# Kernel optimization log

Hardware: AMD Instinct MI355X
Metric: run time of the kernel (lower is better)

## Reference

```python
import jax, jax.numpy as jnp
import numpy as np

N_HEADS = 16
ROPE_BASE = 10000.0


def _apply_rope(t, cos, sin):
    # t: (B, H, S, D); cos/sin: (S, D/2). Rotate-half convention.
    d2 = t.shape[-1] // 2
    t1, t2 = t[..., :d2], t[..., d2:]
    return jnp.concatenate([t1 * cos - t2 * sin, t2 * cos + t1 * sin], axis=-1)


def setup_inputs() -> dict:
    key = jax.random.key(0)
    k0, k1, k2, k3, k4 = jax.random.split(key, 5)
    B, S, E = 4, 2048, 1024
    scale = 0.02
    x = jax.random.normal(k0, (B, S, E), dtype=jnp.float32)
    w_qkv = jax.random.normal(k1, (E, 3 * E), dtype=jnp.float32) * scale
    b_qkv = jnp.zeros((3 * E,), dtype=jnp.float32)
    w_proj = jax.random.normal(k2, (E, E), dtype=jnp.float32) * scale
    b_proj = jnp.zeros((E,), dtype=jnp.float32)
    return {"x": x, "w_qkv": w_qkv, "b_qkv": b_qkv, "w_proj": w_proj, "b_proj": b_proj}


def reference(x, w_qkv, b_qkv, w_proj, b_proj):
    B, S, E = x.shape
    H = N_HEADS
    D = E // H
    # fused QKV projection
    qkv = x @ w_qkv + b_qkv                      # (B, S, 3E)
    q, k, v = jnp.split(qkv, 3, axis=-1)
    def to_heads(t):
        return t.reshape(B, S, H, D).transpose(0, 2, 1, 3)  # (B, H, S, D)
    q, k, v = to_heads(q), to_heads(k), to_heads(v)
    # RoPE (rotate-half)
    inv_freq = ROPE_BASE ** (-jnp.arange(0, D, 2, dtype=jnp.float32) / D)  # (D/2,)
    pos = jnp.arange(S, dtype=jnp.float32)
    freqs = pos[:, None] * inv_freq[None, :]     # (S, D/2)
    cos, sin = jnp.cos(freqs), jnp.sin(freqs)
    q = _apply_rope(q, cos, sin)
    k = _apply_rope(k, cos, sin)
    # causal SDPA
    scores = jnp.einsum('bhqd,bhkd->bhqk', q, k) / jnp.sqrt(jnp.float32(D))
    causal = jnp.tril(jnp.ones((S, S), dtype=bool))
    scores = jnp.where(causal, scores, jnp.float32(-1e30))
    probs = jax.nn.softmax(scores, axis=-1)
    out = jnp.einsum('bhqk,bhkd->bhqd', probs, v)  # (B, H, S, D)
    out = out.transpose(0, 2, 1, 3).reshape(B, S, E)
    # output projection (dropout is identity at p=0 / eval)
    return out @ w_proj + b_proj
```

## Files before the change

kernel.cpp:

```cpp
#include <hip/hip_runtime.h>

typedef unsigned short u16;
typedef __bf16 bf16x8 __attribute__((ext_vector_type(8)));
typedef float f32x4 __attribute__((ext_vector_type(4)));

__device__ __forceinline__ u16 f2b(float f) {
    unsigned u = __builtin_bit_cast(unsigned, f);
    unsigned r = (u + 0x7fffu + ((u >> 16) & 1u)) >> 16;
    return (u16)r;
}
#if __has_builtin(__builtin_amdgcn_cvt_pk_bf16_f32)
typedef __bf16 bf16x2_t __attribute__((ext_vector_type(2)));
__device__ __forceinline__ unsigned pk2(float a, float b) {
    return __builtin_bit_cast(unsigned, __builtin_amdgcn_cvt_pk_bf16_f32(a, b));
}
#else
__device__ __forceinline__ unsigned pk2(float a, float b) {
    return (unsigned)f2b(a) | ((unsigned)f2b(b) << 16);
}
#endif
#if __has_builtin(__builtin_amdgcn_exp2f)
#define EXP2F(x) __builtin_amdgcn_exp2f(x)
#else
#define EXP2F(x) exp2f(x)
#endif

__device__ __forceinline__ void gl_lds16(const u16* g, u16* l) {
    __builtin_amdgcn_global_load_lds(
        (const __attribute__((address_space(1))) unsigned*)(const void*)g,
        (__attribute__((address_space(3))) unsigned*)(void*)l, 16, 0, 0);
}

__device__ __forceinline__ void transpose64(const float* __restrict__ in,
                                            u16* __restrict__ out, int R, int C,
                                            int tr, int tc, int tid, u16 (*tile)[66]) {
    for (int i = tid; i < 4096; i += 256) {
        int r = i >> 6, c = i & 63;
        tile[c][r] = f2b(in[(size_t)(tr + r) * C + tc + c]);
    }
    __syncthreads();
    for (int i = tid; i < 4096; i += 256) {
        int r = i >> 6, c = i & 63;
        out[(size_t)(tc + r) * R + tr + c] = tile[r][c];
    }
}

__global__ __launch_bounds__(256) void k_prep(const float* __restrict__ x,
                                              u16* __restrict__ x_bf,
                                              const float* __restrict__ w_qkv,
                                              u16* __restrict__ wqkvT,
                                              const float* __restrict__ w_proj,
                                              u16* __restrict__ wprojT,
                                              float2* __restrict__ tab) {
    __shared__ u16 tile[64][66];
    int bid = blockIdx.x, tid = threadIdx.x;
    if (bid < 4096) {
        int i = bid * 256 + tid;
        const float4* p = (const float4*)(x + (size_t)i * 8);
        float4 a = p[0], b = p[1];
        u16 t[8] = {f2b(a.x), f2b(a.y), f2b(a.z), f2b(a.w),
                    f2b(b.x), f2b(b.y), f2b(b.z), f2b(b.w)};
        *(uint4*)(x_bf + (size_t)i * 8) = *(const uint4*)t;
    } else if (bid < 4864) {
        int q = bid - 4096;
        transpose64(w_qkv, wqkvT, 1024, 3072, (q / 48) * 64, (q % 48) * 64, tid, tile);
    } else if (bid < 5120) {
        int q = bid - 4864;
        transpose64(w_proj, wprojT, 1024, 1024, (q / 16) * 64, (q % 16) * 64, tid, tile);
    } else {
        int i = (bid - 5120) * 256 + tid;
        int s = i >> 5, d = i & 31;
        const float C0 = 0.4152410118609203f;
        float inv_freq = exp2f(-C0 * (float)d);
        float sn, cs;
        sincosf((float)s * inv_freq, &sn, &cs);
        tab[i] = make_float2(cs, sn);
    }
}

__device__ __forceinline__ void gemm_mainloop(const u16* __restrict__ Ab,
                                              const u16* __restrict__ Bb, int K,
                                              u16* As, u16* Bs, int tid,
                                              f32x4 (&acc)[4][4]) {
    const int wave = tid >> 6, lane = tid & 63;
    const int col = lane & 15, quad = lane >> 4;
    const int wm = wave >> 1, wn = wave & 1;
    const int lrow = lane >> 2, lk = (lane & 3) * 8;
    u16* ldsA0 = As + (wave * 16) * 32;
    u16* ldsA1 = As + (64 + wave * 16) * 32;
    u16* ldsB0 = Bs + (wave * 16) * 32;
    u16* ldsB1 = Bs + (64 + wave * 16) * 32;
    const u16* gA0 = Ab + (size_t)(wave * 16 + lrow) * K + lk;
    const u16* gA1 = gA0 + (size_t)64 * K;
    const u16* gB0 = Bb + (size_t)(wave * 16 + lrow) * K + lk;
    const u16* gB1 = gB0 + (size_t)64 * K;
    for (int k0 = 0; k0 < K; k0 += 64) {
        if (k0) __syncthreads();
#pragma unroll
        for (int kh = 0; kh < 2; ++kh) {
            int ko = k0 + kh * 32;
            gl_lds16(gA0 + ko, ldsA0 + kh * 4096);
            gl_lds16(gA1 + ko, ldsA1 + kh * 4096);
            gl_lds16(gB0 + ko, ldsB0 + kh * 4096);
            gl_lds16(gB1 + ko, ldsB1 + kh * 4096);
        }
        __syncthreads();
#pragma unroll
        for (int kh = 0; kh < 2; ++kh) {
            bf16x8 af[4], bfr[4];
#pragma unroll
            for (int mt = 0; mt < 4; ++mt)
                af[mt] = *(const bf16x8*)(As + kh * 4096 +
                                          (wm * 64 + mt * 16 + col) * 32 + quad * 8);
#pragma unroll
            for (int nt = 0; nt < 4; ++nt)
                bfr[nt] = *(const bf16x8*)(Bs + kh * 4096 +
                                           (wn * 64 + nt * 16 + col) * 32 + quad * 8);
#pragma unroll
            for (int mt = 0; mt < 4; ++mt)
#pragma unroll
                for (int nt = 0; nt < 4; ++nt)
                    acc[mt][nt] = __builtin_amdgcn_mfma_f32_16x16x32_bf16(
                        af[mt], bfr[nt], acc[mt][nt], 0, 0, 0);
        }
    }
}

__global__ __launch_bounds__(256) void k_gemm_qkv_rope(
    const u16* __restrict__ A, const u16* __restrict__ Bt,
    const float* __restrict__ bias, const float2* __restrict__ tab,
    u16* __restrict__ Qr, u16* __restrict__ Kr, u16* __restrict__ Vt) {
    __shared__ __align__(16) u16 smem[16384];
    u16* As = smem;
    u16* Bs = smem + 8192;
    const int K = 1024;
    int tid = threadIdx.x;
    int lane = tid & 63, wave = tid >> 6;
    int col = lane & 15, quad = lane >> 4;
    int wm = wave >> 1, wn = wave & 1;
    int mBase = blockIdx.y * 128;
    int nBase = blockIdx.x * 128;
    f32x4 acc[4][4] = {};
    gemm_mainloop(A + (size_t)mBase * K, Bt + (size_t)nBase * K, K, As, Bs, tid, acc);

    int region = nBase >> 10;
    int n64 = nBase + wn * 64;
    int h = (n64 & 1023) >> 6;
    if (region < 2) {
        __syncthreads();
        float qs = (region == 0) ? 0.18033688011112042f : 1.0f;
#pragma unroll
        for (int nt = 0; nt < 2; ++nt) {
            int d1 = nt * 16 + col;
            float b1 = bias[n64 + d1];
            float b2 = bias[n64 + d1 + 32];
            int nl = wn * 64 + nt * 16 + col;
#pragma unroll
            for (int mt = 0; mt < 4; ++mt) {
                int mlb = wm * 64 + mt * 16 + quad * 4;
#pragma unroll
                for (int r = 0; r < 4; ++r) {
                    int mloc = mlb + r;
                    int s = (mBase + mloc) & 2047;
                    float2 t = tab[s * 32 + d1];
                    float t1 = acc[mt][nt][r] + b1;
                    float t2 = acc[mt][nt + 2][r] + b2;
                    int sw = (mloc & 7) << 3;
                    smem[mloc * 128 + (nl ^ sw)] = f2b((t1 * t.x - t2 * t.y) * qs);
                    smem[mloc * 128 + ((nl + 32) ^ sw)] = f2b((t2 * t.x + t1 * t.y) * qs);
                }
            }
        }
        __syncthreads();
        u16* outp = (region == 0) ? Qr : Kr;
#pragma unroll
        for (int p = 0; p < 8; ++p) {
            int lin = p * 256 + tid;
            int mloc = lin >> 4;
            int c8 = (lin & 15) << 3;
            uint4 v = *(const uint4*)(smem + mloc * 128 + (c8 ^ ((mloc & 7) << 3)));
            int m = mBase + mloc;
            int s = m & 2047, b = m >> 11;
            int ng = (nBase & 1023) + c8;
            *(uint4*)(outp + ((size_t)((b * 16 + (ng >> 6)) * 2048 + s)) * 64 +
                      (ng & 63)) = v;
        }
    } else {
        int b = mBase >> 11;
        int sb0 = mBase & 2047;
#pragma unroll
        for (int nt = 0; nt < 4; ++nt) {
            int d = nt * 16 + col;
            float bv = bias[n64 + d];
            u16* vrow = Vt + ((size_t)((b * 16 + h) * 64 + d)) * 2048;
#pragma unroll
            for (int mt = 0; mt < 4; ++mt) {
                int s = sb0 + wm * 64 + mt * 16 + quad * 4;
                uint2 w;
                w.x = pk2(acc[mt][nt][0] + bv, acc[mt][nt][1] + bv);
                w.y = pk2(acc[mt][nt][2] + bv, acc[mt][nt][3] + bv);
                *(uint2*)(vrow + s) = w;
            }
        }
    }
}

__device__ __forceinline__ void stage_kv(const u16* __restrict__ Kt,
                                         const u16* __restrict__ Vtb, u16* KsB,
                                         u16* VsB, int wave, int lane) {
    int lr = lane >> 3;
    int lc = lane & 7;
#pragma unroll
    for (int i = 0; i < 2; ++i) {
        int s = wave * 2 + i;
        int r = s * 8 + lr;
        int key = (r & 3) | (((r >> 3) & 1) << 2);
        gl_lds16(Kt + (size_t)r * 64 + ((lc ^ key) << 3), KsB + s * 512);
    }
#pragma unroll
    for (int i = 0; i < 2; ++i) {
        int s = wave * 2 + i;
        int d = s * 8 + lr;
        int key = d & 7;
        gl_lds16(Vtb + (size_t)d * 2048 + ((lc ^ key) << 3), VsB + s * 512);
    }
}

__global__ __launch_bounds__(256, 4) void k_attn(const u16* __restrict__ Qr,
                                                 const u16* __restrict__ Kr,
                                                 const u16* __restrict__ Vt,
                                                 u16* __restrict__ O) {
    __shared__ __align__(16) u16 Ks[2][4096];
    __shared__ __align__(16) u16 Vs[2][4096];
    int tid = threadIdx.x, wave = tid >> 6, lane = tid & 63;
    int col = lane & 15, quad = lane >> 4;
    int id = blockIdx.x + (blockIdx.y << 4);
    int xcd = id & 7, w = id >> 3;
    int head = xcd * 8 + (w & 7);
    int tsel = w >> 3;
    int b = head >> 4, h = head & 15;
    size_t headQ = (size_t)head * 2048 * 64;
    size_t headV = (size_t)head * 64 * 2048;
    int prow = (col >> 2) * 8 + (col & 3);
    int ck = col & 7;

#pragma unroll 1
    for (int phase = 0; phase < 2; ++phase) {
        int T = phase ? tsel : 31 - tsel;
        int myq = T * 64 + wave * 16 + col;
        const u16* qp = Qr + headQ + (size_t)myq * 64;
        bf16x8 aq0 = *(const bf16x8*)(qp + quad * 8);
        bf16x8 aq1 = *(const bf16x8*)(qp + 32 + quad * 8);
        f32x4 o[4] = {};
        float l = 0.f;

        stage_kv(Kr + headQ, Vt + headV, Ks[0], Vs[0], wave, lane);
        __syncthreads();

        for (int j = 0; j <= T; ++j) {
            int cur = j & 1;
            if (j < T)
                stage_kv(Kr + headQ + ((size_t)(j + 1) << 12),
                         Vt + headV + (j + 1) * 64, Ks[cur ^ 1], Vs[cur ^ 1],
                         wave, lane);
            const u16* KsC = Ks[cur];
            const u16* VsC = Vs[cur];
            f32x4 s[4];
            __builtin_amdgcn_s_setprio(1);
#pragma unroll
            for (int nt = 0; nt < 4; ++nt) {
                const u16* kp = KsC + ((nt & 1) * 32 + (nt >> 1) * 4 + prow) * 64;
                bf16x8 ak0 = *(const bf16x8*)(kp + ((quad ^ ck) << 3));
                bf16x8 ak1 = *(const bf16x8*)(kp + (((quad + 4) ^ ck) << 3));
                f32x4 z = {};
                z = __builtin_amdgcn_mfma_f32_16x16x32_bf16(ak0, aq0, z, 0, 0, 0);
                s[nt] = __builtin_amdgcn_mfma_f32_16x16x32_bf16(ak1, aq1, z, 0, 0, 0);
            }
            __builtin_amdgcn_s_setprio(0);
            if (j == T) {
#pragma unroll
                for (int nt = 0; nt < 4; ++nt) {
                    int keyb = j * 64 + (nt & 1) * 32 + quad * 8 + (nt >> 1) * 4;
#pragma unroll
                    for (int r = 0; r < 4; ++r)
                        if (keyb + r > myq) s[nt][r] = -3.0e38f;
                }
            }
            unsigned P4[8];
#pragma unroll
            for (int nt = 0; nt < 4; ++nt) {
                float p0 = EXP2F(s[nt][0]);
                float p1 = EXP2F(s[nt][1]);
                float p2 = EXP2F(s[nt][2]);
                float p3 = EXP2F(s[nt][3]);
                l += (p0 + p1) + (p2 + p3);
                P4[2 * nt] = pk2(p0, p1);
                P4[2 * nt + 1] = pk2(p2, p3);
            }
            __builtin_amdgcn_s_setprio(1);
#pragma unroll
            for (int kk = 0; kk < 2; ++kk) {
                uint4 bw;
                bw.x = P4[2 * kk];
                bw.y = P4[2 * kk + 1];
                bw.z = P4[2 * kk + 4];
                bw.w = P4[2 * kk + 5];
                bf16x8 bp = __builtin_bit_cast(bf16x8, bw);
#pragma unroll
                for (int mt = 0; mt < 4; ++mt) {
                    bf16x8 av = *(const bf16x8*)(VsC + (mt * 16 + col) * 64 +
                                                 (((kk * 4 + quad) ^ ck) << 3));
                    o[mt] = __builtin_amdgcn_mfma_f32_16x16x32_bf16(av, bp, o[mt], 0, 0, 0);
                }
            }
            __builtin_amdgcn_s_setprio(0);
            __syncthreads();
        }
        l += __shfl_xor(l, 16);
        l += __shfl_xor(l, 32);
        float inv = 1.0f / l;
        u16* orow = O + (size_t)(b * 2048 + myq) * 1024 + h * 64;
#pragma unroll
        for (int mt = 0; mt < 4; ++mt) {
            uint2 w2;
            w2.x = pk2(o[mt][0] * inv, o[mt][1] * inv);
            w2.y = pk2(o[mt][2] * inv, o[mt][3] * inv);
            *(uint2*)(orow + mt * 16 + quad * 4) = w2;
        }
    }
}

__device__ __forceinline__ void proj_mainloop(const u16* __restrict__ Ab,
                                              const u16* __restrict__ Bb,
                                              u16* As, u16* Bs, int tid,
                                              f32x4 (&acc)[2][4]) {
    const int wave = tid >> 6, lane = tid & 63;
    const int col = lane & 15, quad = lane >> 4;
    const int lrow = lane >> 2, lk = (lane & 3) * 8;
    u16* ldsA0 = As + (wave * 16) * 32;
    u16* ldsA1 = As + (64 + wave * 16) * 32;
    u16* ldsB0 = Bs + (wave * 16) * 32;
    const u16* gA0 = Ab + (size_t)(wave * 16 + lrow) * 1024 + lk;
    const u16* gA1 = gA0 + (size_t)64 * 1024;
    const u16* gB0 = Bb + (size_t)(wave * 16 + lrow) * 1024 + lk;
    for (int k0 = 0; k0 < 1024; k0 += 64) {
        if (k0) __syncthreads();
#pragma unroll
        for (int kh = 0; kh < 2; ++kh) {
            int ko = k0 + kh * 32;
            gl_lds16(gA0 + ko, ldsA0 + kh * 4096);
            gl_lds16(gA1 + ko, ldsA1 + kh * 4096);
            gl_lds16(gB0 + ko, ldsB0 + kh * 2048);
        }
        __syncthreads();
#pragma unroll
        for (int kh = 0; kh < 2; ++kh) {
            bf16x8 af[2], bfr[4];
#pragma unroll
            for (int mt = 0; mt < 2; ++mt)
                af[mt] = *(const bf16x8*)(As + kh * 4096 +
                                          (wave * 32 + mt * 16 + col) * 32 + quad * 8);
#pragma unroll
            for (int nt = 0; nt < 4; ++nt)
                bfr[nt] = *(const bf16x8*)(Bs + kh * 2048 +
                                           (nt * 16 + col) * 32 + quad * 8);
#pragma unroll
            for (int mt = 0; mt < 2; ++mt)
#pragma unroll
                for (int nt = 0; nt < 4; ++nt)
                    acc[mt][nt] = __builtin_amdgcn_mfma_f32_16x16x32_bf16(
                        af[mt], bfr[nt], acc[mt][nt], 0, 0, 0);
        }
    }
}

__global__ __launch_bounds__(256, 4) void k_gemm_proj(const u16* __restrict__ A,
                                                      const u16* __restrict__ Bt,
                                                      const float* __restrict__ bias,
                                                      float* __restrict__ out) {
    __shared__ __align__(16) u16 As[2 * 128 * 32];
    __shared__ __align__(16) u16 Bs[2 * 64 * 32];
    int tid = threadIdx.x;
    int lane = tid & 63, wave = tid >> 6;
    int col = lane & 15, quad = lane >> 4;
    int mBase = blockIdx.y * 128;
    int nBase = blockIdx.x * 64;
    f32x4 acc[2][4] = {};
    proj_mainloop(A + (size_t)mBase * 1024, Bt + (size_t)nBase * 1024, As, Bs, tid, acc);
#pragma unroll
    for (int nt = 0; nt < 4; ++nt) {
        int n = nBase + nt * 16 + col;
        float bv = bias[n];
#pragma unroll
        for (int mt = 0; mt < 2; ++mt) {
            int m = mBase + wave * 32 + mt * 16 + quad * 4;
#pragma unroll
            for (int r = 0; r < 4; ++r)
                out[(size_t)(m + r) * 1024 + n] = acc[mt][nt][r] + bv;
        }
    }
}

extern "C" void kernel_launch(void* const* d_in, const int* in_sizes, int n_in,
                              void* d_out, int out_size, void* d_ws, size_t ws_size,
                              hipStream_t stream) {
    const float* x = (const float*)d_in[0];
    const float* w_qkv = (const float*)d_in[1];
    const float* b_qkv = (const float*)d_in[2];
    const float* w_proj = (const float*)d_in[3];
    const float* b_proj = (const float*)d_in[4];
    float* out = (float*)d_out;
    char* ws = (char*)d_ws;
    u16* x_bf = (u16*)(ws);
    u16* wqkvT = (u16*)(ws + 16777216);
    u16* wprojT = (u16*)(ws + 23068672);
    u16* Qr = (u16*)(ws + 25165824);
    u16* Kr = (u16*)(ws + 41943040);
    u16* Vt = (u16*)(ws + 58720256);
    u16* AO = (u16*)(ws + 75497472);
    float2* tab = (float2*)(ws + 75497472);

    k_prep<<<5376, 256, 0, stream>>>(x, x_bf, w_qkv, wqkvT, w_proj, wprojT, tab);
    k_gemm_qkv_rope<<<dim3(24, 64), 256, 0, stream>>>(x_bf, wqkvT, b_qkv, tab, Qr, Kr, Vt);
    k_attn<<<dim3(16, 64), 256, 0, stream>>>(Qr, Kr, Vt, AO);
    k_gemm_proj<<<dim3(16, 64), 256, 0, stream>>>(AO, wprojT, b_proj, out);
}
```

Baseline: 254.3 us.

## Triple-buffer K tiles in attention and replace syncthreads with vmcnt-gated barriers

Splits the K/V staging helper into separate K and V loaders and grows the K LDS buffer from two to three slots, so K is prefetched two tiles ahead while V stays one tile ahead. Full __syncthreads is replaced by explicit s_waitcnt vmcnt counts plus raw s_barrier and sched_barrier. The V wait now sits just before the PV MFMAs, so the QK and softmax work can overlap the outstanding V loads. This adds LDS use, which may lower occupancy. The V wait only covers each wave's own global-to-LDS loads and has no barrier before other waves read them, so there is a cross-wave race risk.

```diff
diff --git a/kernel.cpp b/kernel.cpp
--- a/kernel.cpp
+++ b/kernel.cpp
@@ -205,11 +205,9 @@
     }
 }
 
-__device__ __forceinline__ void stage_kv(const u16* __restrict__ Kt,
-                                         const u16* __restrict__ Vtb, u16* KsB,
-                                         u16* VsB, int wave, int lane) {
-    int lr = lane >> 3;
-    int lc = lane & 7;
+__device__ __forceinline__ void stage_k(const u16* __restrict__ Kt, u16* KsB,
+                                        int wave, int lane) {
+    int lr = lane >> 3, lc = lane & 7;
 #pragma unroll
     for (int i = 0; i < 2; ++i) {
         int s = wave * 2 + i;
@@ -217,6 +215,10 @@
         int key = (r & 3) | (((r >> 3) & 1) << 2);
         gl_lds16(Kt + (size_t)r * 64 + ((lc ^ key) << 3), KsB + s * 512);
     }
+}
+__device__ __forceinline__ void stage_v(const u16* __restrict__ Vtb, u16* VsB,
+                                        int wave, int lane) {
+    int lr = lane >> 3, lc = lane & 7;
 #pragma unroll
     for (int i = 0; i < 2; ++i) {
         int s = wave * 2 + i;
@@ -230,7 +232,7 @@
                                                  const u16* __restrict__ Kr,
                                                  const u16* __restrict__ Vt,
                                                  u16* __restrict__ O) {
-    __shared__ __align__(16) u16 Ks[2][4096];
+    __shared__ __align__(16) u16 Ks[3][4096];
     __shared__ __align__(16) u16 Vs[2][4096];
     int tid = threadIdx.x, wave = tid >> 6, lane = tid & 63;
     int col = lane & 15, quad = lane >> 4;
@@ -243,6 +245,8 @@
     size_t headV = (size_t)head * 64 * 2048;
     int prow = (col >> 2) * 8 + (col & 3);
     int ck = col & 7;
+    const u16* Kh = Kr + headQ;
+    const u16* Vh = Vt + headV;
 
 #pragma unroll 1
     for (int phase = 0; phase < 2; ++phase) {
@@ -254,17 +258,23 @@
         f32x4 o[4] = {};
         float l = 0.f;
 
-        stage_kv(Kr + headQ, Vt + headV, Ks[0], Vs[0], wave, lane);
-        __syncthreads();
-
+        stage_k(Kh, Ks[0], wave, lane);
+        stage_v(Vh, Vs[0], wave, lane);
+        stage_k(Kh + (1 << 12), Ks[1], wave, lane);
+        asm volatile("s_waitcnt vmcnt(2)" ::: "memory");
+        __builtin_amdgcn_s_barrier();
+        __builtin_amdgcn_sched_barrier(0);
+
+        int kcur = 0;
         for (int j = 0; j <= T; ++j) {
-            int cur = j & 1;
-            if (j < T)
-                stage_kv(Kr + headQ + ((size_t)(j + 1) << 12),
-                         Vt + headV + (j + 1) * 64, Ks[cur ^ 1], Vs[cur ^ 1],
-                         wave, lane);
-            const u16* KsC = Ks[cur];
-            const u16* VsC = Vs[cur];
+            bool pfK = (j + 2 <= T);
+            bool pfV = (j + 1 <= T);
+            if (pfK)
+                stage_k(Kh + ((size_t)(j + 2) << 12), Ks[kcur == 0 ? 2 : kcur - 1],
+                        wave, lane);
+            if (pfV) stage_v(Vh + (j + 1) * 64, Vs[(j + 1) & 1], wave, lane);
+            const u16* KsC = Ks[kcur];
+            const u16* VsC = Vs[j & 1];
             f32x4 s[4];
             __builtin_amdgcn_s_setprio(1);
 #pragma unroll
@@ -297,6 +307,13 @@
                 P4[2 * nt] = pk2(p0, p1);
                 P4[2 * nt + 1] = pk2(p2, p3);
             }
+            if (pfK)
+                asm volatile("s_waitcnt vmcnt(4)" ::: "memory");
+            else if (pfV)
+                asm volatile("s_waitcnt vmcnt(2)" ::: "memory");
+            else
+                asm volatile("s_waitcnt vmcnt(0)" ::: "memory");
+            __builtin_amdgcn_sched_barrier(0);
             __builtin_amdgcn_s_setprio(1);
 #pragma unroll
             for (int kk = 0; kk < 2; ++kk) {
@@ -314,7 +331,9 @@
                 }
             }
             __builtin_amdgcn_s_setprio(0);
-            __syncthreads();
+            __builtin_amdgcn_s_barrier();
+            __builtin_amdgcn_sched_barrier(0);
+            kcur = (kcur == 2) ? 0 : kcur + 1;
         }
         l += __shfl_xor(l, 16);
         l += __shfl_xor(l, 32);
```

Result: no change. 251.4 us (-1.1%).
